# Kernel tuning notes

Hardware: AMD Instinct MI355X
Metric: run time of the kernel (lower is better)

## Reference

```python
import jax, jax.numpy as jnp
import numpy as np

PIXEL_THRESHOLD = 0.4
FRACTION_THRESHOLD = 0.03
NUM_CLASSES = 20
N, H, W = 100, 640, 960
LOGIT_SCALE = 8.0  # makes the instance-axis softmax peaky enough to cross PIXEL_THRESHOLD


def setup_inputs() -> dict:
    key = jax.random.key(0)
    k1, k2, k3 = jax.random.split(key, 3)
    cls_prob = jax.random.uniform(k1, (N,), dtype=jnp.float32)
    mask_prob = jax.random.normal(k2, (N, H, W), dtype=jnp.float32) * LOGIT_SCALE
    cls_idx = jax.random.randint(k3, (N,), 0, NUM_CLASSES)
    return {"cls_prob": cls_prob, "mask_prob": mask_prob, "cls_idx": cls_idx}


def _mask_removal(cls_prob, mask_prob, cls_idx):
    # Sort instances by class confidence, descending (greedy NMS order).
    order = jnp.argsort(-cls_prob)
    cls_prob_s = cls_prob[order]          # [N]
    cls_idx_s = cls_idx[order]            # [N]
    raw_s = mask_prob[order]              # [N,H,W] pre-softmax logits (mask_prob_copy)
    # Per-pixel softmax over the instance axis (permutation-equivariant, so
    # softmax-then-sort == sort-then-softmax as in the original).
    sm = jax.nn.softmax(raw_s, axis=0)    # [N,H,W]

    def step(state, inp):
        panoptic, mask_image = state      # [H,W], [C,H,W]
        smi, rawi, ci = inp
        logit = (smi >= PIXEL_THRESHOLD).astype(rawi.dtype)   # binarized mask [H,W]
        mask_sum = logit.sum()
        curr = mask_image[ci]
        overlap = jnp.sum((curr >= 1.0) & (logit == 1.0)).astype(rawi.dtype) / jnp.maximum(mask_sum, 1.0)
        degenerate = (logit.max() == logit.min()) | (mask_sum == 0.0)
        skip = degenerate | (overlap > FRACTION_THRESHOLD)
        # assign only unclaimed panoptic pixels inside the binarized mask
        assign = (panoptic == 0.0) & (logit == 1.0) & jnp.logical_not(skip)
        keep_mask = jnp.where(assign, rawi, 0.0)              # use_mask_low_constant=False
        panoptic = jnp.where(assign, 1.0, panoptic)
        mask_image = mask_image.at[ci].add(jnp.where(assign, logit, 0.0))
        return (panoptic, mask_image), (keep_mask, jnp.logical_not(skip))

    init = (jnp.zeros((H, W), jnp.float32), jnp.zeros((NUM_CLASSES, H, W), jnp.float32))
    _, (keep_masks, keep_flags) = jax.lax.scan(step, init, (sm, raw_s, cls_idx_s))
    # Fixed-shape outputs: keep_flags marks which (sorted) instances survived;
    # dropped instances have all-zero keep_masks rows.
    return cls_prob_s, keep_masks, cls_idx_s, keep_flags


def reference(cls_prob, mask_prob, cls_idx):
    return _mask_removal(cls_prob, mask_prob, cls_idx)
```

## Files before the change

kernel.cpp:

```cpp
#include <hip/hip_runtime.h>
#include <cstdint>
#include <cstddef>

#define N_INST 100
#define HW (640 * 960)
#define PIX_THR 0.4f
#define FRAC_THR 0.03f
#define EPS_BORDER 5e-5f
#define FLAG_CAP 65536
#define L2E 1.4426950408889634f

#define CB 1200
#define ZB 480
#define GRID (CB + ZB)
#define CHUNK_F4 15360
#define CHUNK_ITER 120
#define NCHUNK 1000
#define FIN_BLOCKS 128

#define OUT_MASKS_OFF 100
#define OUT_CLSIDX_OFF (100 + (size_t)N_INST * HW)
#define OUT_FLAGS_OFF (100 + (size_t)N_INST * HW + N_INST)


__global__ __launch_bounds__(256) void k0_init(
    const float* __restrict__ cls_prob,
    const int* __restrict__ cls_idx,
    int* __restrict__ ord,
    int* __restrict__ rank_arr,
    float* __restrict__ out,
    unsigned* __restrict__ mask_sum,
    unsigned* __restrict__ ctrs,
    unsigned* __restrict__ pair_cnt) {
    int t = threadIdx.x;
    if (t < N_INST) {
        float pi = cls_prob[t];
        int rank = 0;
        for (int j = 0; j < N_INST; ++j) {
            float pj = cls_prob[j];
            rank += (pj > pi) || (pj == pi && j < t);
        }
        ord[rank] = t;
        rank_arr[t] = rank;
        out[rank] = pi;
        out[OUT_CLSIDX_OFF + rank] = (float)cls_idx[t];
        mask_sum[t] = 0u;
    }
    if (t < 3) ctrs[t] = 0u;
    for (int i = t; i < N_INST * N_INST; i += 256)
        pair_cnt[i] = 0u;
}

__global__ __launch_bounds__(128) void k1_fused(
    const float* __restrict__ mask,
    const int* __restrict__ rank_arr,
    unsigned* __restrict__ mask_sum,
    unsigned* __restrict__ pair_cnt,
    uint4* __restrict__ pvals,
    unsigned* __restrict__ flag_count,
    unsigned* __restrict__ flag_list,
    unsigned* __restrict__ zctr,
    float* __restrict__ out) {
    int t = threadIdx.x;

    if (blockIdx.x < CB) {
        __shared__ int srank[N_INST];
        __shared__ unsigned ssum[N_INST];
        if (t < N_INST) {
            srank[t] = rank_arr[t];
            ssum[t] = 0u;
        }
        __syncthreads();

        int p0 = (blockIdx.x * 128 + t) * 4;
        const float* base = mask + p0;

        float S[4] = {0.0f, 0.0f, 0.0f, 0.0f};
        float m[4] = {-3.4e38f, -3.4e38f, -3.4e38f, -3.4e38f};
        float n[4] = {-3.4e38f, -3.4e38f, -3.4e38f, -3.4e38f};
        int ia[4] = {0, 0, 0, 0};
        int ib[4] = {0, 0, 0, 0};

#pragma unroll 10
        for (int i = 0; i < N_INST; ++i) {
            float4 v4 = *(const float4*)(base + (size_t)i * HW);
            float vv[4] = {v4.x, v4.y, v4.z, v4.w};
#pragma unroll
            for (int j = 0; j < 4; ++j) {
                float v = vv[j];
                S[j] += exp2f(v * L2E);
                bool gt = v > m[j];
                bool g2 = v > n[j];
                n[j] = fmaxf(n[j], fminf(m[j], v));
                ib[j] = gt ? ia[j] : (g2 ? i : ib[j]);
                ia[j] = gt ? i : ia[j];
                m[j] = fmaxf(m[j], v);
            }
        }

#pragma unroll
        for (int j = 0; j < 4; ++j) {
            int p = p0 + j;
            float e1 = exp2f(m[j] * L2E);
            float e2 = exp2f(n[j] * L2E);
            float t04 = 0.4f * S[j];
            float w = EPS_BORDER * S[j];
            bool q1 = e1 >= t04;
            bool border = (fabsf(e1 - t04) < w) || (q1 && fabsf(e2 - t04) < w);

            unsigned c = 0u;
            float vlo = 0.0f, vhi = 0.0f;
            if (border) {
                unsigned slot = atomicAdd(flag_count, 1u);
                if (slot < FLAG_CAP) flag_list[slot] = (unsigned)p;
            } else if (q1) {
                bool q2 = e2 >= t04;
                int r1 = srank[ia[j]];
                atomicAdd(&ssum[r1], 1u);
                if (q2) {
                    int r2 = srank[ib[j]];
                    atomicAdd(&ssum[r2], 1u);
                    int lo = min(r1, r2), hi = max(r1, r2);
                    atomicAdd(&pair_cnt[lo * N_INST + hi], 1u);
                    c = (unsigned)(lo + 1) | ((unsigned)(hi + 1) << 8);
                    vlo = (r1 < r2) ? m[j] : n[j];
                    vhi = (r1 < r2) ? n[j] : m[j];
                } else {
                    c = (unsigned)(r1 + 1);
                    vlo = m[j];
                }
            }
            pvals[p] = make_uint4(c, __float_as_uint(vlo), __float_as_uint(vhi), 0u);
        }

        __syncthreads();
        if (t < N_INST && ssum[t] != 0u)
            atomicAdd(&mask_sum[t], ssum[t]);
        return;
    }

    __shared__ unsigned s_chunk;
    for (;;) {
        if (t == 0) s_chunk = atomicAdd(zctr, 1u);
        __syncthreads();
        unsigned c = s_chunk;
        __syncthreads();
        if (c >= NCHUNK) break;
        float4* dst = (float4*)(out + OUT_MASKS_OFF) + (size_t)c * CHUNK_F4 + t;
        const float4 z4 = make_float4(0.0f, 0.0f, 0.0f, 0.0f);
#pragma unroll 8
        for (int k = 0; k < CHUNK_ITER; ++k)
            dst[k * 128] = z4;
    }
}

__global__ __launch_bounds__(256) void k2_finish(
    const float* __restrict__ mask,
    const int* __restrict__ ord,
    const int* __restrict__ cls_idx,
    unsigned* __restrict__ mask_sum,
    unsigned* __restrict__ pair_cnt,
    uint4* __restrict__ pvals,
    const unsigned* __restrict__ flag_count,
    const unsigned* __restrict__ flag_list,
    unsigned* __restrict__ done,
    int* __restrict__ keep,
    float* __restrict__ out) {
    __shared__ int sord[N_INST];
    __shared__ unsigned s_last;
    int t = threadIdx.x;
    if (t < N_INST) sord[t] = ord[t];
    __syncthreads();

    unsigned nf = *flag_count;
    if (nf > FLAG_CAP) nf = FLAG_CAP;
    for (unsigned idx = blockIdx.x * 256 + t; idx < nf;
         idx += FIN_BLOCKS * 256) {
        int p = (int)flag_list[idx];
        float v[N_INST];
#pragma unroll
        for (int i = 0; i < N_INST; ++i)
            v[i] = mask[(size_t)sord[i] * HW + p];

        float m = v[0];
        int p1 = 0;
        float m2 = -3.4e38f;
        int p2 = 0;
#pragma unroll
        for (int i = 1; i < N_INST; ++i) {
            if (v[i] > m) { m2 = m; p2 = p1; m = v[i]; p1 = i; }
            else if (v[i] > m2) { m2 = v[i]; p2 = i; }
        }
        float d = 0.0f;
#pragma unroll
        for (int i = 0; i < N_INST; ++i)
            d += expf(v[i] - m);

        float sm1 = 1.0f / d;
        float sm2 = expf(m2 - m) / d;
        bool q1 = (sm1 >= PIX_THR);
        bool q2 = (sm2 >= PIX_THR);
        unsigned c = 0u;
        float vlo = 0.0f, vhi = 0.0f;
        if (q1) {
            atomicAdd(&mask_sum[p1], 1u);
            if (q2) {
                atomicAdd(&mask_sum[p2], 1u);
                int lo = min(p1, p2), hi = max(p1, p2);
                atomicAdd(&pair_cnt[lo * N_INST + hi], 1u);
                c = (unsigned)(lo + 1) | ((unsigned)(hi + 1) << 8);
                vlo = v[lo];
                vhi = v[hi];
            } else {
                c = (unsigned)(p1 + 1);
                vlo = v[p1];
            }
        }
        pvals[p] = make_uint4(c, __float_as_uint(vlo), __float_as_uint(vhi), 0u);
    }

    __threadfence();
    if (t == 0) s_last = atomicAdd(done, 1u);
    __syncthreads();
    if (s_last != FIN_BLOCKS - 1) return;
    __threadfence();

    __shared__ unsigned spair[N_INST * N_INST];
    __shared__ int scls[N_INST];
    __shared__ unsigned sms[N_INST];
    __shared__ int skeep[N_INST];
    for (int i = t; i < N_INST * N_INST; i += 256)
        spair[i] = pair_cnt[i];
    if (t < N_INST) {
        scls[t] = cls_idx[sord[t]];
        sms[t] = mask_sum[t];
    }
    __syncthreads();

    for (int b = 0; b < N_INST; ++b) {
        if (t < 64) {
            unsigned cnt = 0u;
            for (int a = t; a < b; a += 64)
                if (skeep[a] && scls[a] == scls[b])
                    cnt += spair[a * N_INST + b];
#pragma unroll
            for (int off = 32; off; off >>= 1)
                cnt += __shfl_down((int)cnt, off);
            if (t == 0) {
                unsigned ms = sms[b];
                float overlap = (float)cnt / fmaxf((float)ms, 1.0f);
                bool degen = (ms == 0u) || (ms == (unsigned)HW);
                bool skip = degen || (overlap > FRAC_THR);
                skeep[b] = skip ? 0 : 1;
            }
        }
        __syncthreads();
    }

    if (t < N_INST) {
        keep[t] = skeep[t];
        out[OUT_FLAGS_OFF + t] = (float)skeep[t];
    }
}

__global__ __launch_bounds__(256) void k3_scatter(
    const uint4* __restrict__ pvals,
    const int* __restrict__ keep,
    float* __restrict__ out) {
    __shared__ int skeep[N_INST];
    if (threadIdx.x < N_INST) skeep[threadIdx.x] = keep[threadIdx.x];
    __syncthreads();

    int p = blockIdx.x * 256 + threadIdx.x;
    uint4 pv = pvals[p];
    unsigned c = pv.x;
    if (c == 0u) return;
    int a = (int)(c & 0xFFu) - 1;
    int b = (int)(c >> 8) - 1;

    int inst;
    float val;
    if (skeep[a]) {
        inst = a;
        val = __uint_as_float(pv.y);
    } else if (b >= 0 && skeep[b]) {
        inst = b;
        val = __uint_as_float(pv.z);
    } else {
        return;
    }
    out[OUT_MASKS_OFF + (size_t)inst * HW + p] = val;
}

extern "C" void kernel_launch(void* const* d_in, const int* in_sizes, int n_in,
                              void* d_out, int out_size, void* d_ws, size_t ws_size,
                              hipStream_t stream) {
    const float* cls_prob = (const float*)d_in[0];
    const float* mask = (const float*)d_in[1];
    const int* cls_idx = (const int*)d_in[2];
    float* out = (float*)d_out;

    char* ws = (char*)d_ws;
    int* ord = (int*)(ws + 0);
    int* rank_arr = (int*)(ws + 512);
    int* keep = (int*)(ws + 1024);
    unsigned* mask_sum = (unsigned*)(ws + 1536);
    unsigned* ctrs = (unsigned*)(ws + 2048);
    unsigned* pair_cnt = (unsigned*)(ws + 4096);
    uint4* pvals = (uint4*)(ws + 65536);
    unsigned* flag_list = (unsigned*)(ws + 65536 + (size_t)HW * 16);

    unsigned* flag_count = &ctrs[0];
    unsigned* zctr = &ctrs[1];
    unsigned* done = &ctrs[2];

    k0_init<<<1, 256, 0, stream>>>(cls_prob, cls_idx, ord, rank_arr, out,
                                   mask_sum, ctrs, pair_cnt);
    k1_fused<<<GRID, 128, 0, stream>>>(mask, rank_arr, mask_sum, pair_cnt,
                                       pvals, flag_count, flag_list, zctr, out);
    k2_finish<<<FIN_BLOCKS, 256, 0, stream>>>(mask, ord, cls_idx, mask_sum,
                                              pair_cnt, pvals, flag_count,
                                              flag_list, done, keep, out);
    k3_scatter<<<HW / 256, 256, 0, stream>>>(pvals, keep, out);
}
```

Baseline: 253.8 us.

## Fuse scatter into finish kernel with spin-wait flag; nontemporal zero stores

The separate k3_scatter launch is folded into k2_finish. The last-arriving block runs the sequential keep scan and then sets a global flag, while the other 127 blocks spin on that flag before all blocks scatter kept mask values in a grid-stride loop. The zero-fill of the output masks now uses nontemporal vector stores to avoid polluting cache. This saves one kernel launch and its tail, but relies on all 128 blocks being co-resident for the spin-wait to be safe, and the scatter now runs on only 128 blocks instead of 2400.

```diff
diff --git a/kernel.cpp b/kernel.cpp
--- a/kernel.cpp
+++ b/kernel.cpp
@@ -17,6 +17,8 @@
 #define CHUNK_ITER 120
 #define NCHUNK 1000
 #define FIN_BLOCKS 128
+
+typedef float f4_t __attribute__((ext_vector_type(4)));
 
 #define OUT_MASKS_OFF 100
 #define OUT_CLSIDX_OFF (100 + (size_t)N_INST * HW)
@@ -46,7 +48,7 @@
         out[OUT_CLSIDX_OFF + rank] = (float)cls_idx[t];
         mask_sum[t] = 0u;
     }
-    if (t < 3) ctrs[t] = 0u;
+    if (t < 4) ctrs[t] = 0u;
     for (int i = t; i < N_INST * N_INST; i += 256)
         pair_cnt[i] = 0u;
 }
@@ -146,11 +148,11 @@
         unsigned c = s_chunk;
         __syncthreads();
         if (c >= NCHUNK) break;
-        float4* dst = (float4*)(out + OUT_MASKS_OFF) + (size_t)c * CHUNK_F4 + t;
-        const float4 z4 = make_float4(0.0f, 0.0f, 0.0f, 0.0f);
+        f4_t* dst = (f4_t*)(out + OUT_MASKS_OFF) + (size_t)c * CHUNK_F4 + t;
+        const f4_t z4 = {0.0f, 0.0f, 0.0f, 0.0f};
 #pragma unroll 8
         for (int k = 0; k < CHUNK_ITER; ++k)
-            dst[k * 128] = z4;
+            __builtin_nontemporal_store(z4, &dst[k * 128]);
     }
 }
 
@@ -164,10 +166,12 @@
     const unsigned* __restrict__ flag_count,
     const unsigned* __restrict__ flag_list,
     unsigned* __restrict__ done,
+    unsigned* __restrict__ scan_flag,
     int* __restrict__ keep,
     float* __restrict__ out) {
     __shared__ int sord[N_INST];
     __shared__ unsigned s_last;
+    __shared__ int skp[N_INST];
     int t = threadIdx.x;
     if (t < N_INST) sord[t] = ord[t];
     __syncthreads();
@@ -222,74 +226,78 @@
     __threadfence();
     if (t == 0) s_last = atomicAdd(done, 1u);
     __syncthreads();
-    if (s_last != FIN_BLOCKS - 1) return;
-    __threadfence();
-
-    __shared__ unsigned spair[N_INST * N_INST];
-    __shared__ int scls[N_INST];
-    __shared__ unsigned sms[N_INST];
-    __shared__ int skeep[N_INST];
-    for (int i = t; i < N_INST * N_INST; i += 256)
-        spair[i] = pair_cnt[i];
-    if (t < N_INST) {
-        scls[t] = cls_idx[sord[t]];
-        sms[t] = mask_sum[t];
-    }
-    __syncthreads();
-
-    for (int b = 0; b < N_INST; ++b) {
-        if (t < 64) {
-            unsigned cnt = 0u;
-            for (int a = t; a < b; a += 64)
-                if (skeep[a] && scls[a] == scls[b])
-                    cnt += spair[a * N_INST + b];
-#pragma unroll
-            for (int off = 32; off; off >>= 1)
-                cnt += __shfl_down((int)cnt, off);
-            if (t == 0) {
-                unsigned ms = sms[b];
-                float overlap = (float)cnt / fmaxf((float)ms, 1.0f);
-                bool degen = (ms == 0u) || (ms == (unsigned)HW);
-                bool skip = degen || (overlap > FRAC_THR);
-                skeep[b] = skip ? 0 : 1;
+
+    if (s_last == FIN_BLOCKS - 1) {
+        __threadfence();
+
+        __shared__ unsigned spair[N_INST * N_INST];
+        __shared__ int scls[N_INST];
+        __shared__ unsigned sms[N_INST];
+        for (int i = t; i < N_INST * N_INST; i += 256)
+            spair[i] = pair_cnt[i];
+        if (t < N_INST) {
+            scls[t] = cls_idx[sord[t]];
+            sms[t] = mask_sum[t];
+        }
+        __syncthreads();
+
+        for (int b = 0; b < N_INST; ++b) {
+            if (t < 64) {
+                unsigned cnt = 0u;
+                for (int a = t; a < b; a += 64)
+                    if (skp[a] && scls[a] == scls[b])
+                        cnt += spair[a * N_INST + b];
+#pragma unroll
+                for (int off = 32; off; off >>= 1)
+                    cnt += __shfl_down((int)cnt, off);
+                if (t == 0) {
+                    unsigned ms = sms[b];
+                    float overlap = (float)cnt / fmaxf((float)ms, 1.0f);
+                    bool degen = (ms == 0u) || (ms == (unsigned)HW);
+                    bool skip = degen || (overlap > FRAC_THR);
+                    skp[b] = skip ? 0 : 1;
+                }
             }
-        }
-        __syncthreads();
-    }
-
-    if (t < N_INST) {
-        keep[t] = skeep[t];
-        out[OUT_FLAGS_OFF + t] = (float)skeep[t];
-    }
-}
-
-__global__ __launch_bounds__(256) void k3_scatter(
-    const uint4* __restrict__ pvals,
-    const int* __restrict__ keep,
-    float* __restrict__ out) {
-    __shared__ int skeep[N_INST];
-    if (threadIdx.x < N_INST) skeep[threadIdx.x] = keep[threadIdx.x];
-    __syncthreads();
-
-    int p = blockIdx.x * 256 + threadIdx.x;
-    uint4 pv = pvals[p];
-    unsigned c = pv.x;
-    if (c == 0u) return;
-    int a = (int)(c & 0xFFu) - 1;
-    int b = (int)(c >> 8) - 1;
-
-    int inst;
-    float val;
-    if (skeep[a]) {
-        inst = a;
-        val = __uint_as_float(pv.y);
-    } else if (b >= 0 && skeep[b]) {
-        inst = b;
-        val = __uint_as_float(pv.z);
+            __syncthreads();
+        }
+
+        if (t < N_INST) {
+            keep[t] = skp[t];
+            out[OUT_FLAGS_OFF + t] = (float)skp[t];
+        }
+        __threadfence();
+        __syncthreads();
+        if (t == 0) atomicExch(scan_flag, 1u);
     } else {
-        return;
-    }
-    out[OUT_MASKS_OFF + (size_t)inst * HW + p] = val;
+        if (t == 0) {
+            while (atomicAdd(scan_flag, 0u) == 0u)
+                __builtin_amdgcn_s_sleep(8);
+        }
+        __syncthreads();
+        __threadfence();
+        if (t < N_INST) skp[t] = atomicAdd((int*)&keep[t], 0);
+        __syncthreads();
+    }
+
+    for (int p = blockIdx.x * 256 + t; p < HW; p += FIN_BLOCKS * 256) {
+        uint4 pv = pvals[p];
+        unsigned c = pv.x;
+        if (c == 0u) continue;
+        int a = (int)(c & 0xFFu) - 1;
+        int b = (int)(c >> 8) - 1;
+        int inst;
+        float val;
+        if (skp[a]) {
+            inst = a;
+            val = __uint_as_float(pv.y);
+        } else if (b >= 0 && skp[b]) {
+            inst = b;
+            val = __uint_as_float(pv.z);
+        } else {
+            continue;
+        }
+        out[OUT_MASKS_OFF + (size_t)inst * HW + p] = val;
+    }
 }
 
 extern "C" void kernel_launch(void* const* d_in, const int* in_sizes, int n_in,
@@ -313,6 +321,7 @@
     unsigned* flag_count = &ctrs[0];
     unsigned* zctr = &ctrs[1];
     unsigned* done = &ctrs[2];
+    unsigned* scan_flag = &ctrs[3];
 
     k0_init<<<1, 256, 0, stream>>>(cls_prob, cls_idx, ord, rank_arr, out,
                                    mask_sum, ctrs, pair_cnt);
@@ -320,6 +329,6 @@
                                        pvals, flag_count, flag_list, zctr, out);
     k2_finish<<<FIN_BLOCKS, 256, 0, stream>>>(mask, ord, cls_idx, mask_sum,
                                               pair_cnt, pvals, flag_count,
-                                              flag_list, done, keep, out);
-    k3_scatter<<<HW / 256, 256, 0, stream>>>(pvals, keep, out);
+                                              flag_list, done, scan_flag,
+                                              keep, out);
 }
```

After: 260.4 us. +2.6%, slower.
